# Performance work log

Hardware: AMD Instinct MI355X
Metric: run time of the kernel (lower is better)

The kernel has to match this reference:

```python
import jax, jax.numpy as jnp
import numpy as np

N_NODES = 100000
N_EDGES = 1600000
NUM_GRAPHS = 128
EPS = 1e-5


def setup_inputs() -> dict:
    key = jax.random.key(0)
    ks = jax.random.split(key, 8)
    x = jax.random.normal(ks[0], (N_NODES, 8), dtype=jnp.float32)
    edge_index = jax.random.randint(ks[1], (2, N_EDGES), 0, N_NODES, dtype=jnp.int64)
    batch = jnp.sort(jax.random.randint(ks[2], (N_NODES,), 0, NUM_GRAPHS, dtype=jnp.int64))
    W1_l = jax.random.normal(ks[3], (128, 8), dtype=jnp.float32) * 0.3
    b1 = jnp.zeros((128,), dtype=jnp.float32)
    W1_r = jax.random.normal(ks[4], (128, 8), dtype=jnp.float32) * 0.3
    g1 = jnp.ones((128,), dtype=jnp.float32)
    beta1 = jnp.zeros((128,), dtype=jnp.float32)
    W2_l = jax.random.normal(ks[5], (128, 128), dtype=jnp.float32) * 0.08
    b2 = jnp.zeros((128,), dtype=jnp.float32)
    W2_r = jax.random.normal(ks[6], (128, 128), dtype=jnp.float32) * 0.08
    g2 = jnp.ones((128,), dtype=jnp.float32)
    beta2 = jnp.zeros((128,), dtype=jnp.float32)
    return dict(x=x, edge_index=edge_index, batch=batch,
                W1_l=W1_l, b1=b1, W1_r=W1_r, g1=g1, beta1=beta1,
                W2_l=W2_l, b2=b2, W2_r=W2_r, g2=g2, beta2=beta2)


def _sage_conv(x, src, dst, W_l, b, W_r):
    # PyG SAGEConv: out = lin_l(mean_j x_j) + lin_r(x_i); lin_r has no bias
    msg = x[src]                                              # [E, F]
    agg = jax.ops.segment_sum(msg, dst, num_segments=N_NODES)
    deg = jax.ops.segment_sum(jnp.ones((src.shape[0],), x.dtype), dst,
                              num_segments=N_NODES)
    agg = agg / jnp.maximum(deg, 1.0)[:, None]                # mean aggregation
    return agg @ W_l.T + b + x @ W_r.T


def _batch_norm(h, gamma, beta):
    # training-mode BN over the node dimension
    mu = jnp.mean(h, axis=0)
    var = jnp.mean(jnp.square(h - mu), axis=0)
    return gamma * (h - mu) * jax.lax.rsqrt(var + EPS) + beta


def reference(x, edge_index, batch, W1_l, b1, W1_r, g1, beta1,
              W2_l, b2, W2_r, g2, beta2):
    src, dst = edge_index[0], edge_index[1]
    x1 = jax.nn.relu(_batch_norm(_sage_conv(x, src, dst, W1_l, b1, W1_r), g1, beta1))
    x2 = jax.nn.relu(_batch_norm(_sage_conv(x1, src, dst, W2_l, b2, W2_r), g2, beta2))
    h = x1 + x2  # dropout is identity in eval mode
    # global mean pool per graph
    s = jax.ops.segment_sum(h, batch, num_segments=NUM_GRAPHS)
    cnt = jax.ops.segment_sum(jnp.ones((h.shape[0],), h.dtype), batch,
                              num_segments=NUM_GRAPHS)
    return s / jnp.maximum(cnt, 1.0)[:, None]                 # [NUM_GRAPHS, 128]
```

## Files before the change

### kernel.cpp

```cpp
#include <hip/hip_runtime.h>
#include <cstdint>
#include <cstddef>

namespace {

constexpr int N_NODES = 100000;
constexpr int N_EDGES = 1600000;
constexpr int NUM_GRAPHS = 128;
constexpr int F = 128;
constexpr float BN_EPS = 1e-5f;

constexpr int W_BUCK = 512;
constexpr int NBUCK = (N_NODES + W_BUCK - 1) / W_BUCK;
constexpr int CB = 400;
constexpr int CHUNK = N_EDGES / CB;

typedef float f32x4 __attribute__((ext_vector_type(4)));
typedef float f32x2 __attribute__((ext_vector_type(2)));
typedef short s16x8 __attribute__((ext_vector_type(8)));
typedef unsigned char uchar;
union B8 { uint4 u; s16x8 s; };

__device__ inline ushort f2bf(float x) {
    uint u = __float_as_uint(x);
    u += 0x7fffu + ((u >> 16) & 1u);
    return (ushort)(u >> 16);
}
__device__ inline float bf2f(ushort s) { return __uint_as_float(((uint)s) << 16); }
__device__ inline uint pack2(float lo, float hi) {
    return (uint)f2bf(lo) | ((uint)f2bf(hi) << 16);
}
__device__ inline float bflo(uint u) { return __uint_as_float(u << 16); }
__device__ inline float bfhi(uint u) { return __uint_as_float(u & 0xffff0000u); }

__device__ inline void acc4f8(float* a, uint u) {
    f32x2 lo = __builtin_amdgcn_cvt_pk_f32_fp8((int)u, false);
    f32x2 hi = __builtin_amdgcn_cvt_pk_f32_fp8((int)u, true);
    a[0] += lo[0]; a[1] += lo[1]; a[2] += hi[0]; a[3] += hi[1];
}
__device__ inline void acc8bf(float* a, uint4 v) {
    a[0] += bflo(v.x); a[1] += bfhi(v.x);
    a[2] += bflo(v.y); a[3] += bfhi(v.y);
    a[4] += bflo(v.z); a[5] += bfhi(v.z);
    a[6] += bflo(v.w); a[7] += bfhi(v.w);
}


constexpr int PB_HIST  = CB;
constexpr int PB_BOUND = (N_NODES + 255) / 256;
constexpr int PB_PB    = 64;
constexpr int PB_PB1   = 16;
constexpr int PB_PX    = (N_NODES + 255) / 256;
constexpr int PB_Z     = (512 + NUM_GRAPHS * F) / 256;
constexpr int PB_TOTAL = PB_HIST + PB_BOUND + PB_PB + PB_PB1 + PB_PX + PB_Z;

__global__ void __launch_bounds__(256) k_pre(
        const int* __restrict__ ei, int* __restrict__ gcount,
        const int* __restrict__ batch, int* __restrict__ gstart,
        const float* __restrict__ W2l, const float* __restrict__ W2r,
        ushort* __restrict__ Wcat,
        const float* __restrict__ W1l, const float* __restrict__ W1r,
        ushort* __restrict__ Wcat1,
        const float* __restrict__ x, ushort* __restrict__ xbf,
        float* __restrict__ stats, float* __restrict__ outacc) {
    __shared__ int bins[NBUCK];
    int bid = blockIdx.x, t = threadIdx.x;
    if (bid < PB_HIST) {
        for (int i = t; i < NBUCK; i += 256) bins[i] = 0;
        __syncthreads();
        int e0 = bid * CHUNK;
        for (int i = t; i < CHUNK; i += 256)
            atomicAdd(&bins[ei[N_EDGES + e0 + i] >> 9], 1);
        __syncthreads();
        for (int i = t; i < NBUCK; i += 256) gcount[i * CB + bid] = bins[i];
        return;
    }
    bid -= PB_HIST;
    if (bid < PB_BOUND) {
        int i = bid * 256 + t;
        if (i >= N_NODES) return;
        int b = batch[i];
        if (i == 0) {
            for (int g = 0; g <= b; ++g) gstart[g] = 0;
        } else {
            int p = batch[i - 1];
            if (p != b) for (int g = p + 1; g <= b; ++g) gstart[g] = i;
        }
        if (i == N_NODES - 1) {
            for (int g = b + 1; g <= NUM_GRAPHS; ++g) gstart[g] = N_NODES;
        }
        return;
    }
    bid -= PB_BOUND;
    if (bid < PB_PB) {
        int i = bid * 256 + t;
        int f = i >> 7, k = i & 127;
        Wcat[f * 256 + k]       = f2bf(W2l[i]);
        Wcat[f * 256 + 128 + k] = f2bf(W2r[i]);
        return;
    }
    bid -= PB_PB;
    if (bid < PB_PB1) {
        int i = bid * 256 + t;
        int f = i >> 5, k = i & 31;
        float v = (k < 8) ? W1r[f * 8 + k] : ((k < 16) ? W1l[f * 8 + (k - 8)] : 0.f);
        Wcat1[i] = f2bf(v);
        return;
    }
    bid -= PB_PB1;
    if (bid < PB_PX) {
        int n = bid * 256 + t;
        if (n >= N_NODES) return;
        const float4* xp = (const float4*)(x + (size_t)n * 8);
        float4 x0 = xp[0], x1 = xp[1];
        uint4 o = {pack2(x0.x, x0.y), pack2(x0.z, x0.w),
                   pack2(x1.x, x1.y), pack2(x1.z, x1.w)};
        *(uint4*)(xbf + (size_t)n * 8) = o;
        return;
    }
    bid -= PB_PX;
    {
        int i = bid * 256 + t;
        if (i < 512) stats[i] = 0.f;
        else outacc[i - 512] = 0.f;
    }
}


__global__ void __launch_bounds__(512) k_scanA(int* __restrict__ g,
                                               int* __restrict__ bsum) {
    __shared__ int tmp[512];
    int b = blockIdx.x, t = threadIdx.x;
    int v = (t < CB) ? g[b * CB + t] : 0;
    tmp[t] = v;
    __syncthreads();
    #pragma unroll
    for (int d = 1; d < 512; d <<= 1) {
        int u = (t >= d) ? tmp[t - d] : 0;
        __syncthreads();
        tmp[t] += u;
        __syncthreads();
    }
    if (t < CB) g[b * CB + t] = tmp[t] - v;
    if (t == 511) bsum[b] = tmp[511];
}

__global__ void __launch_bounds__(256) k_part(const int* __restrict__ ei,
                                              const int* __restrict__ gloc,
                                              const int* __restrict__ bsum,
                                              uint* __restrict__ epk) {
    __shared__ int cur[NBUCK];
    __shared__ int pref[256];
    int t = threadIdx.x;
    int v = (t < NBUCK) ? bsum[t] : 0;
    pref[t] = v;
    __syncthreads();
    #pragma unroll
    for (int d = 1; d < 256; d <<= 1) {
        int u = (t >= d) ? pref[t - d] : 0;
        __syncthreads();
        pref[t] += u;
        __syncthreads();
    }
    if (t < NBUCK) cur[t] = gloc[t * CB + blockIdx.x] + (pref[t] - v);
    __syncthreads();
    int e0 = blockIdx.x * CHUNK;
    for (int i = t; i < CHUNK; i += 256) {
        int d = ei[N_EDGES + e0 + i];
        int s = ei[e0 + i];
        int p = atomicAdd(&cur[d >> 9], 1);
        epk[p] = ((uint)s << 9) | (uint)(d & 511);
    }
}

__global__ void __launch_bounds__(512) k_rank(const uint* __restrict__ epk,
                                              const int* __restrict__ bsum,
                                              int* __restrict__ offs,
                                              int* __restrict__ ssrc,
                                              const float* __restrict__ x,
                                              const ushort* __restrict__ xbf,
                                              ushort* __restrict__ xa) {
    __shared__ int dcnt[W_BUCK];
    __shared__ int tmp[W_BUCK];
    __shared__ int cur[W_BUCK];
    __shared__ int pref[256];
    int b = blockIdx.x, t = threadIdx.x;
    if (t < 256) pref[t] = (t < NBUCK) ? bsum[t] : 0;
    __syncthreads();
    #pragma unroll
    for (int d = 1; d < 256; d <<= 1) {
        int u = (t < 256 && t >= d) ? pref[t - d] : 0;
        __syncthreads();
        if (t < 256) pref[t] += u;
        __syncthreads();
    }
    int s0 = pref[b] - bsum[b];
    int s1 = pref[b];
    dcnt[t] = 0;
    __syncthreads();
    for (int i = s0 + t; i < s1; i += 512)
        atomicAdd(&dcnt[epk[i] & 511u], 1);
    __syncthreads();
    int v = dcnt[t];
    tmp[t] = v;
    __syncthreads();
    #pragma unroll
    for (int d = 1; d < 512; d <<= 1) {
        int u = (t >= d) ? tmp[t - d] : 0;
        __syncthreads();
        tmp[t] += u;
        __syncthreads();
    }
    int start = s0 + tmp[t] - v;
    int node = b * W_BUCK + t;
    if (node <= N_NODES) offs[node] = start;
    cur[t] = start;
    __syncthreads();
    for (int i = s0 + t; i < s1; i += 512) {
        uint u = epk[i];
        int p = atomicAdd(&cur[u & 511u], 1);
        ssrc[p] = (int)(u >> 9);
    }

    __syncthreads();
    if (node >= N_NODES) return;
    int gs = start, ge = start + v;
    float a[8];
    #pragma unroll
    for (int i = 0; i < 8; ++i) a[i] = 0.f;
    int j = gs;
    for (; j + 7 < ge; j += 8) {
        int i0 = ssrc[j],   i1 = ssrc[j+1], i2 = ssrc[j+2], i3 = ssrc[j+3];
        int i4 = ssrc[j+4], i5 = ssrc[j+5], i6 = ssrc[j+6], i7 = ssrc[j+7];
        uint4 v0 = *(const uint4*)(xbf + (size_t)i0 * 8);
        uint4 v1 = *(const uint4*)(xbf + (size_t)i1 * 8);
        uint4 v2 = *(const uint4*)(xbf + (size_t)i2 * 8);
        uint4 v3 = *(const uint4*)(xbf + (size_t)i3 * 8);
        uint4 v4 = *(const uint4*)(xbf + (size_t)i4 * 8);
        uint4 v5 = *(const uint4*)(xbf + (size_t)i5 * 8);
        uint4 v6 = *(const uint4*)(xbf + (size_t)i6 * 8);
        uint4 v7 = *(const uint4*)(xbf + (size_t)i7 * 8);
        acc8bf(a, v0); acc8bf(a, v1); acc8bf(a, v2); acc8bf(a, v3);
        acc8bf(a, v4); acc8bf(a, v5); acc8bf(a, v6); acc8bf(a, v7);
    }
    for (; j + 3 < ge; j += 4) {
        int i0 = ssrc[j], i1 = ssrc[j+1], i2 = ssrc[j+2], i3 = ssrc[j+3];
        uint4 v0 = *(const uint4*)(xbf + (size_t)i0 * 8);
        uint4 v1 = *(const uint4*)(xbf + (size_t)i1 * 8);
        uint4 v2 = *(const uint4*)(xbf + (size_t)i2 * 8);
        uint4 v3 = *(const uint4*)(xbf + (size_t)i3 * 8);
        acc8bf(a, v0); acc8bf(a, v1); acc8bf(a, v2); acc8bf(a, v3);
    }
    for (; j < ge; ++j)
        acc8bf(a, *(const uint4*)(xbf + (size_t)ssrc[j] * 8));
    int dg = ge - gs;
    float inv = 1.0f / (float)(dg > 1 ? dg : 1);
    const float4* xp = (const float4*)(x + (size_t)node * 8);
    float4 x0 = xp[0], x1v = xp[1];
    ushort* row = xa + (size_t)node * 32;
    uint4 o0 = {pack2(x0.x, x0.y), pack2(x0.z, x0.w), pack2(x1v.x, x1v.y), pack2(x1v.z, x1v.w)};
    uint4 o1 = {pack2(a[0]*inv, a[1]*inv), pack2(a[2]*inv, a[3]*inv),
                pack2(a[4]*inv, a[5]*inv), pack2(a[6]*inv, a[7]*inv)};
    uint4 z = {0u, 0u, 0u, 0u};
    *(uint4*)(row)      = o0;
    *(uint4*)(row + 8)  = o1;
    *(uint4*)(row + 16) = z;
    *(uint4*)(row + 24) = z;
}


__global__ void __launch_bounds__(256) k_lin1(
        const ushort* __restrict__ xa, const ushort* __restrict__ Wcat1,
        const float* __restrict__ b1, ushort* __restrict__ h1bf,
        float* __restrict__ stats) {
    __shared__ ushort sOut[64 * 140];
    __shared__ float sred[256];
    int tid = threadIdx.x;
    int wave = tid >> 6, lane = tid & 63;
    int quad = lane >> 4, l16 = lane & 15;
    int n0 = blockIdx.x * 64;

    int node = n0 + wave * 16 + l16;
    int cn = (node < N_NODES) ? node : N_NODES - 1;
    B8 ta;
    ta.u = *(const uint4*)(xa + (size_t)cn * 32 + quad * 8);

    #pragma unroll
    for (int nt = 0; nt < 8; ++nt) {
        int fb = nt * 16 + l16;
        B8 tb;
        tb.u = *(const uint4*)(Wcat1 + fb * 32 + quad * 8);
        f32x4 acc = {0.f, 0.f, 0.f, 0.f};
        acc = __builtin_amdgcn_mfma_f32_16x16x32_bf16(ta.s, tb.s, acc, 0, 0, 0);
        float bb = b1[fb];
        #pragma unroll
        for (int r = 0; r < 4; ++r) {
            int row = wave * 16 + quad * 4 + r;
            sOut[row * 140 + fb] = f2bf(acc[r] + bb);
        }
    }
    __syncthreads();

    #pragma unroll
    for (int p = 0; p < 4; ++p) {
        int row = p * 16 + (tid >> 4);
        int nd = n0 + row;
        if (nd < N_NODES) {
            int c0 = (tid & 15) * 8;
            uint4 v = *(const uint4*)&sOut[row * 140 + c0];
            *(uint4*)(h1bf + (size_t)nd * F + c0) = v;
        }
    }

    int f = tid & 127, half = tid >> 7;
    float s = 0.f, s2 = 0.f;
    for (int r = half * 32; r < half * 32 + 32; ++r) {
        if (n0 + r >= N_NODES) break;
        float v = bf2f(sOut[r * 140 + f]);
        s += v; s2 += v * v;
    }
    if (half) { sred[f] = s; sred[128 + f] = s2; }
    __syncthreads();
    if (!half) {
        s += sred[f]; s2 += sred[128 + f];
        atomicAdd(&stats[f], s);
        atomicAdd(&stats[F + f], s2);
    }
}

__global__ void k_bnrelu(const ushort* __restrict__ h, const float* __restrict__ stats,
                         const float* __restrict__ gamma, const float* __restrict__ beta,
                         ushort* __restrict__ x1bf, uchar* __restrict__ x1f8) {
    int i = blockIdx.x * 256 + threadIdx.x;
    int base = i * 8;
    int f = base & (F - 1);
    float sc[8], sh[8];
    #pragma unroll
    for (int k = 0; k < 8; ++k) {
        float mu  = stats[f + k] * (1.0f / N_NODES);
        float var = stats[F + f + k] * (1.0f / N_NODES) - mu * mu;
        float s   = gamma[f + k] * rsqrtf(var + BN_EPS);
        sc[k] = s;
        sh[k] = beta[f + k] - mu * s;
    }
    uint4 hv = *(const uint4*)(h + base);
    float v0 = fmaxf(0.f, bflo(hv.x)*sc[0] + sh[0]);
    float v1 = fmaxf(0.f, bfhi(hv.x)*sc[1] + sh[1]);
    float v2 = fmaxf(0.f, bflo(hv.y)*sc[2] + sh[2]);
    float v3 = fmaxf(0.f, bfhi(hv.y)*sc[3] + sh[3]);
    float v4 = fmaxf(0.f, bflo(hv.z)*sc[4] + sh[4]);
    float v5 = fmaxf(0.f, bfhi(hv.z)*sc[5] + sh[5]);
    float v6 = fmaxf(0.f, bflo(hv.w)*sc[6] + sh[6]);
    float v7 = fmaxf(0.f, bfhi(hv.w)*sc[7] + sh[7]);
    uint4 o = {pack2(v0,v1), pack2(v2,v3), pack2(v4,v5), pack2(v6,v7)};
    *(uint4*)(x1bf + base) = o;
    int p0 = __builtin_amdgcn_cvt_pk_fp8_f32(v0, v1, 0, false);
    p0     = __builtin_amdgcn_cvt_pk_fp8_f32(v2, v3, p0, true);
    int p1 = __builtin_amdgcn_cvt_pk_fp8_f32(v4, v5, 0, false);
    p1     = __builtin_amdgcn_cvt_pk_fp8_f32(v6, v7, p1, true);
    uint2 o8 = {(uint)p0, (uint)p1};
    *(uint2*)(x1f8 + base) = o8;
}


__global__ void __launch_bounds__(256) k_agg2(
        const uchar* __restrict__ x1f8, const int* __restrict__ offs,
        const int* __restrict__ ssrc, ushort* __restrict__ agg2bf) {
    int t = threadIdx.x;
    int n = blockIdx.x * 32 + (t >> 3);
    int c16 = (t & 7) * 16;
    int s0 = offs[n], s1 = offs[n + 1];
    float acc[16];
    #pragma unroll
    for (int i = 0; i < 16; ++i) acc[i] = 0.f;
    int j = s0;
    for (; j + 7 < s1; j += 8) {
        int i0 = ssrc[j],   i1 = ssrc[j+1], i2 = ssrc[j+2], i3 = ssrc[j+3];
        int i4 = ssrc[j+4], i5 = ssrc[j+5], i6 = ssrc[j+6], i7 = ssrc[j+7];
        uint4 v0 = *(const uint4*)(x1f8 + (size_t)i0 * F + c16);
        uint4 v1 = *(const uint4*)(x1f8 + (size_t)i1 * F + c16);
        uint4 v2 = *(const uint4*)(x1f8 + (size_t)i2 * F + c16);
        uint4 v3 = *(const uint4*)(x1f8 + (size_t)i3 * F + c16);
        uint4 v4 = *(const uint4*)(x1f8 + (size_t)i4 * F + c16);
        uint4 v5 = *(const uint4*)(x1f8 + (size_t)i5 * F + c16);
        uint4 v6 = *(const uint4*)(x1f8 + (size_t)i6 * F + c16);
        uint4 v7 = *(const uint4*)(x1f8 + (size_t)i7 * F + c16);
        acc4f8(acc, v0.x); acc4f8(acc+4, v0.y); acc4f8(acc+8, v0.z); acc4f8(acc+12, v0.w);
        acc4f8(acc, v1.x); acc4f8(acc+4, v1.y); acc4f8(acc+8, v1.z); acc4f8(acc+12, v1.w);
        acc4f8(acc, v2.x); acc4f8(acc+4, v2.y); acc4f8(acc+8, v2.z); acc4f8(acc+12, v2.w);
        acc4f8(acc, v3.x); acc4f8(acc+4, v3.y); acc4f8(acc+8, v3.z); acc4f8(acc+12, v3.w);
        acc4f8(acc, v4.x); acc4f8(acc+4, v4.y); acc4f8(acc+8, v4.z); acc4f8(acc+12, v4.w);
        acc4f8(acc, v5.x); acc4f8(acc+4, v5.y); acc4f8(acc+8, v5.z); acc4f8(acc+12, v5.w);
        acc4f8(acc, v6.x); acc4f8(acc+4, v6.y); acc4f8(acc+8, v6.z); acc4f8(acc+12, v6.w);
        acc4f8(acc, v7.x); acc4f8(acc+4, v7.y); acc4f8(acc+8, v7.z); acc4f8(acc+12, v7.w);
    }
    for (; j + 3 < s1; j += 4) {
        int i0 = ssrc[j], i1 = ssrc[j+1], i2 = ssrc[j+2], i3 = ssrc[j+3];
        uint4 v0 = *(const uint4*)(x1f8 + (size_t)i0 * F + c16);
        uint4 v1 = *(const uint4*)(x1f8 + (size_t)i1 * F + c16);
        uint4 v2 = *(const uint4*)(x1f8 + (size_t)i2 * F + c16);
        uint4 v3 = *(const uint4*)(x1f8 + (size_t)i3 * F + c16);
        acc4f8(acc, v0.x); acc4f8(acc+4, v0.y); acc4f8(acc+8, v0.z); acc4f8(acc+12, v0.w);
        acc4f8(acc, v1.x); acc4f8(acc+4, v1.y); acc4f8(acc+8, v1.z); acc4f8(acc+12, v1.w);
        acc4f8(acc, v2.x); acc4f8(acc+4, v2.y); acc4f8(acc+8, v2.z); acc4f8(acc+12, v2.w);
        acc4f8(acc, v3.x); acc4f8(acc+4, v3.y); acc4f8(acc+8, v3.z); acc4f8(acc+12, v3.w);
    }
    for (; j < s1; ++j) {
        uint4 v = *(const uint4*)(x1f8 + (size_t)ssrc[j] * F + c16);
        acc4f8(acc, v.x); acc4f8(acc+4, v.y); acc4f8(acc+8, v.z); acc4f8(acc+12, v.w);
    }
    int dg = s1 - s0;
    float inv = 1.0f / (float)(dg > 1 ? dg : 1);
    uint4 o0 = {pack2(acc[0]*inv,  acc[1]*inv),  pack2(acc[2]*inv,  acc[3]*inv),
                pack2(acc[4]*inv,  acc[5]*inv),  pack2(acc[6]*inv,  acc[7]*inv)};
    uint4 o1 = {pack2(acc[8]*inv,  acc[9]*inv),  pack2(acc[10]*inv, acc[11]*inv),
                pack2(acc[12]*inv, acc[13]*inv), pack2(acc[14]*inv, acc[15]*inv)};
    ushort* dst = agg2bf + (size_t)n * F + c16;
    *(uint4*)(dst)     = o0;
    *(uint4*)(dst + 8) = o1;
}

__device__ inline int gSw(int f, int j) { return (f << 5) | ((j + f) & 31); }

__global__ void __launch_bounds__(256, 2) k_lin2(
        const ushort* __restrict__ agg2bf, const ushort* __restrict__ x1bf,
        const ushort* __restrict__ Wcat, const float* __restrict__ b2,
        ushort* __restrict__ h2bf, float* __restrict__ stats) {
    __shared__ ushort sB[2048 * 8];
    int tid = threadIdx.x;
    int wave = tid >> 6, lane = tid & 63;
    int quad = lane >> 4, l16 = lane & 15;

    int bid = blockIdx.x;
    int ng, fh;
    if (bid < 768) {
        int g = bid >> 4, i = bid & 15;
        ng = g * 8 + (i & 7);
        fh = i >> 3;
    } else {
        int idx = bid - 768;
        ng = 384 + (idx >> 1);
        fh = idx & 1;
    }
    int fbase = fh * 64;
    int wf = wave & 1, grp = wave >> 1;
    int f0 = wf * 32 + l16;
    int f1 = f0 + 16;

    #pragma unroll
    for (int it = 0; it < 8; ++it) {
        int c = it * 256 + tid;
        int f = c >> 5, j = c & 31;
        uint4 v = *(const uint4*)(Wcat + ((size_t)(fbase + f) * 32 + j) * 8);
        *(uint4*)&sB[gSw(f, j) * 8] = v;
    }
    __syncthreads();

    float bb0 = b2[fbase + f0], bb1 = b2[fbase + f1];
    float s0 = 0.f, s0q = 0.f, s1 = 0.f, s1q = 0.f;
    int n0 = ng * 256 + grp * 128;

    s16x8 aA[8], aB[8];
    auto loadTile = [&](s16x8* a, int nb) {
        int an = nb + l16;
        if (an >= N_NODES) an = N_NODES - 1;
        #pragma unroll
        for (int ks = 0; ks < 8; ++ks) {
            const ushort* src = (ks < 4) ? agg2bf : x1bf;
            B8 tm;
            tm.u = *(const uint4*)(src + (size_t)an * F + (ks & 3) * 32 + quad * 8);
            a[ks] = tm.s;
        }
    };
    auto computeTile = [&](s16x8* a, int nb) {
        f32x4 acc0 = {0,0,0,0}, acc1 = {0,0,0,0};
        #pragma unroll
        for (int ks = 0; ks < 8; ++ks) {
            int j = (ks << 2) + quad;
            B8 tb0, tb1;
            tb0.u = *(const uint4*)&sB[gSw(f0, j) * 8];
            tb1.u = *(const uint4*)&sB[gSw(f1, j) * 8];
            acc0 = __builtin_amdgcn_mfma_f32_16x16x32_bf16(a[ks], tb0.s, acc0, 0, 0, 0);
            acc1 = __builtin_amdgcn_mfma_f32_16x16x32_bf16(a[ks], tb1.s, acc1, 0, 0, 0);
        }
        #pragma unroll
        for (int r = 0; r < 4; ++r) {
            int node = nb + quad * 4 + r;
            if (node < N_NODES) {
                float v0 = acc0[r] + bb0, v1 = acc1[r] + bb1;
                h2bf[(size_t)node * F + fbase + f0] = f2bf(v0);
                h2bf[(size_t)node * F + fbase + f1] = f2bf(v1);
                s0 += v0; s0q += v0 * v0;
                s1 += v1; s1q += v1 * v1;
            }
        }
    };

    loadTile(aA, n0);
    #pragma unroll 1
    for (int p = 0; p < 4; ++p) {
        int nb = n0 + p * 32;
        loadTile(aB, nb + 16);
        computeTile(aA, nb);
        if (p < 3) loadTile(aA, nb + 32);
        computeTile(aB, nb + 16);
    }

    s0  += __shfl_xor(s0, 16);  s0  += __shfl_xor(s0, 32);
    s0q += __shfl_xor(s0q, 16); s0q += __shfl_xor(s0q, 32);
    s1  += __shfl_xor(s1, 16);  s1  += __shfl_xor(s1, 32);
    s1q += __shfl_xor(s1q, 16); s1q += __shfl_xor(s1q, 32);
    if (quad == 0) {
        atomicAdd(&stats[fbase + f0], s0);
        atomicAdd(&stats[F + fbase + f0], s0q);
        atomicAdd(&stats[fbase + f1], s1);
        atomicAdd(&stats[F + fbase + f1], s1q);
    }
}


__global__ void k_pool(const ushort* __restrict__ x1bf, const ushort* __restrict__ h2bf,
                       const float* __restrict__ stats2, const float* __restrict__ gamma2,
                       const float* __restrict__ beta2, const int* __restrict__ batch,
                       float* __restrict__ outacc) {
    int f = threadIdx.x & 127;
    int half = threadIdx.x >> 7;
    float mu  = stats2[f] * (1.0f / N_NODES);
    float var = stats2[F + f] * (1.0f / N_NODES) - mu * mu;
    float sc  = gamma2[f] * rsqrtf(var + BN_EPS);
    float sh  = beta2[f] - mu * sc;
    int n0 = blockIdx.x * 128 + half * 64;
    if (n0 >= N_NODES) return;
    int n1 = min(n0 + 64, N_NODES);
    float acc = 0.f;
    int curg = batch[n0];
    for (int n = n0; n < n1; ++n) {
        int g = batch[n];
        if (g != curg) {
            atomicAdd(&outacc[curg * F + f], acc);
            acc = 0.f; curg = g;
        }
        float v1 = bf2f(x1bf[(size_t)n * F + f]);
        float v2 = fmaxf(0.f, bf2f(h2bf[(size_t)n * F + f]) * sc + sh);
        acc += v1 + v2;
    }
    atomicAdd(&outacc[curg * F + f], acc);
}

__global__ void k_out(const float* __restrict__ outacc, const int* __restrict__ gstart,
                      float* __restrict__ out) {
    int i = blockIdx.x * 256 + threadIdx.x;
    if (i >= NUM_GRAPHS * F) return;
    int g = i >> 7;
    int c = gstart[g + 1] - gstart[g];
    out[i] = outacc[i] / (float)(c > 1 ? c : 1);
}

}

extern "C" void kernel_launch(void* const* d_in, const int* in_sizes, int n_in,
                              void* d_out, int out_size, void* d_ws, size_t ws_size,
                              hipStream_t stream) {
    const float* x     = (const float*)d_in[0];
    const int*   ei    = (const int*)d_in[1];
    const int*   batch = (const int*)d_in[2];
    const float* W1l   = (const float*)d_in[3];
    const float* b1    = (const float*)d_in[4];
    const float* W1r   = (const float*)d_in[5];
    const float* g1    = (const float*)d_in[6];
    const float* be1   = (const float*)d_in[7];
    const float* W2l   = (const float*)d_in[8];
    const float* b2    = (const float*)d_in[9];
    const float* W2r   = (const float*)d_in[10];
    const float* g2    = (const float*)d_in[11];
    const float* be2   = (const float*)d_in[12];
    float* out = (float*)d_out;

    char* w = (char*)d_ws;
    size_t o = 0;
    auto alloc = [&](size_t bytes) {
        void* p = w + o;
        o += (bytes + 511) & ~(size_t)511;
        return p;
    };
    int*    offs   = (int*)alloc((size_t)(N_NODES + 1) * 4);
    int*    gcount = (int*)alloc((size_t)NBUCK * CB * 4);
    int*    bsum   = (int*)alloc((size_t)NBUCK * 4);
    int*    ssrc   = (int*)alloc((size_t)N_EDGES * 4);
    uint*   epk    = (uint*)alloc((size_t)N_EDGES * 4);
    int*    gstart = (int*)alloc((NUM_GRAPHS + 1) * 4);
    float*  stats  = (float*)alloc(512 * 4);
    ushort* Wcat   = (ushort*)alloc((size_t)F * 256 * 2);
    ushort* Wcat1  = (ushort*)alloc((size_t)F * 32 * 2);
    float*  outacc = (float*)alloc((size_t)NUM_GRAPHS * F * 4);
    ushort* xbf    = (ushort*)alloc((size_t)N_NODES * 8 * 2);
    ushort* xa     = (ushort*)alloc((size_t)N_NODES * 32 * 2);
    ushort* h1bf   = (ushort*)alloc((size_t)N_NODES * F * 2);
    ushort* x1bf   = (ushort*)alloc((size_t)N_NODES * F * 2);
    uchar*  x1f8   = (uchar*)alloc((size_t)N_NODES * F);
    ushort* agg2bf = (ushort*)alloc((size_t)N_NODES * F * 2);
    ushort* h2bf   = (ushort*)alloc((size_t)N_NODES * F * 2);

    k_pre<<<PB_TOTAL, 256, 0, stream>>>(ei, gcount, batch, gstart,
                                        W2l, W2r, Wcat, W1l, W1r, Wcat1,
                                        x, xbf, stats, outacc);

    k_scanA<<<NBUCK, 512, 0, stream>>>(gcount, bsum);
    k_part <<<CB, 256, 0, stream>>>(ei, gcount, bsum, epk);
    k_rank <<<NBUCK, 512, 0, stream>>>(epk, bsum, offs, ssrc, x, xbf, xa);

    k_lin1  <<<(N_NODES + 63) / 64, 256, 0, stream>>>(xa, Wcat1, b1, h1bf, stats);
    k_bnrelu<<<(N_NODES * F / 8) / 256, 256, 0, stream>>>(h1bf, stats, g1, be1,
                                                          x1bf, x1f8);

    k_agg2  <<<N_NODES / 32, 256, 0, stream>>>(x1f8, offs, ssrc, agg2bf);
    k_lin2  <<<((N_NODES + 255) / 256) * 2, 256, 0, stream>>>(agg2bf, x1bf, Wcat, b2,
                                                              h2bf, stats + 256);

    k_pool<<<(N_NODES + 127) / 128, 256, 0, stream>>>(x1bf, h2bf, stats + 256,
                                                      g2, be2, batch, outacc);
    k_out <<<(NUM_GRAPHS * F + 255) / 256, 256, 0, stream>>>(outacc, gstart, out);
}
```

Measured before the change: 308.2 us.

## Recompute layer-1 linear to fuse BN+ReLU and drop h1 intermediate buffer

Splits layer-1 linear into a stats-only pass and a second pass that recomputes the cheap K=32 MFMA, then applies BN, ReLU and the bf16/fp8 conversion directly. This removes the write and re-read of the 25.6MB bf16 h1 intermediate and the separate k_bnrelu kernel. It trades that memory traffic for a second read of xa and a duplicated matmul, plus shared-memory atomics for the stats reduction.

```diff
diff --git a/kernel.cpp b/kernel.cpp
--- a/kernel.cpp
+++ b/kernel.cpp
@@ -269,16 +269,16 @@
 }
 
 
-__global__ void __launch_bounds__(256) k_lin1(
+__global__ void __launch_bounds__(256) k_lin1s(
         const ushort* __restrict__ xa, const ushort* __restrict__ Wcat1,
-        const float* __restrict__ b1, ushort* __restrict__ h1bf,
-        float* __restrict__ stats) {
-    __shared__ ushort sOut[64 * 140];
+        const float* __restrict__ b1, float* __restrict__ stats) {
     __shared__ float sred[256];
     int tid = threadIdx.x;
     int wave = tid >> 6, lane = tid & 63;
     int quad = lane >> 4, l16 = lane & 15;
     int n0 = blockIdx.x * 64;
+    sred[tid] = 0.f;
+    __syncthreads();
 
     int node = n0 + wave * 16 + l16;
     int cn = (node < N_NODES) ? node : N_NODES - 1;
@@ -293,10 +293,60 @@
         f32x4 acc = {0.f, 0.f, 0.f, 0.f};
         acc = __builtin_amdgcn_mfma_f32_16x16x32_bf16(ta.s, tb.s, acc, 0, 0, 0);
         float bb = b1[fb];
+        float ls = 0.f, lq = 0.f;
+        #pragma unroll
+        for (int r = 0; r < 4; ++r) {
+            int rn = n0 + wave * 16 + quad * 4 + r;
+            if (rn < N_NODES) {
+                float v = bf2f(f2bf(acc[r] + bb));
+                ls += v; lq += v * v;
+            }
+        }
+        ls += __shfl_xor(ls, 16); ls += __shfl_xor(ls, 32);
+        lq += __shfl_xor(lq, 16); lq += __shfl_xor(lq, 32);
+        if (quad == 0) {
+            atomicAdd(&sred[fb], ls);
+            atomicAdd(&sred[128 + fb], lq);
+        }
+    }
+    __syncthreads();
+    atomicAdd(&stats[tid], sred[tid]);
+}
+
+__global__ void __launch_bounds__(256) k_lin1b(
+        const ushort* __restrict__ xa, const ushort* __restrict__ Wcat1,
+        const float* __restrict__ b1, const float* __restrict__ stats,
+        const float* __restrict__ gamma, const float* __restrict__ beta,
+        ushort* __restrict__ x1bf, uchar* __restrict__ x1f8) {
+    __shared__ ushort sOut[64 * 140];
+    int tid = threadIdx.x;
+    int wave = tid >> 6, lane = tid & 63;
+    int quad = lane >> 4, l16 = lane & 15;
+    int n0 = blockIdx.x * 64;
+
+    int node = n0 + wave * 16 + l16;
+    int cn = (node < N_NODES) ? node : N_NODES - 1;
+    B8 ta;
+    ta.u = *(const uint4*)(xa + (size_t)cn * 32 + quad * 8);
+
+    #pragma unroll
+    for (int nt = 0; nt < 8; ++nt) {
+        int fb = nt * 16 + l16;
+        B8 tb;
+        tb.u = *(const uint4*)(Wcat1 + fb * 32 + quad * 8);
+        f32x4 acc = {0.f, 0.f, 0.f, 0.f};
+        acc = __builtin_amdgcn_mfma_f32_16x16x32_bf16(ta.s, tb.s, acc, 0, 0, 0);
+        float bb = b1[fb];
+        float mu  = stats[fb] * (1.0f / N_NODES);
+        float var = stats[F + fb] * (1.0f / N_NODES) - mu * mu;
+        float sc  = gamma[fb] * rsqrtf(var + BN_EPS);
+        float sh  = beta[fb] - mu * sc;
         #pragma unroll
         for (int r = 0; r < 4; ++r) {
             int row = wave * 16 + quad * 4 + r;
-            sOut[row * 140 + fb] = f2bf(acc[r] + bb);
+            float v = bf2f(f2bf(acc[r] + bb));
+            float y = fmaxf(0.f, v * sc + sh);
+            sOut[row * 140 + fb] = f2bf(y);
         }
     }
     __syncthreads();
@@ -308,58 +358,17 @@
         if (nd < N_NODES) {
             int c0 = (tid & 15) * 8;
             uint4 v = *(const uint4*)&sOut[row * 140 + c0];
-            *(uint4*)(h1bf + (size_t)nd * F + c0) = v;
-        }
-    }
-
-    int f = tid & 127, half = tid >> 7;
-    float s = 0.f, s2 = 0.f;
-    for (int r = half * 32; r < half * 32 + 32; ++r) {
-        if (n0 + r >= N_NODES) break;
-        float v = bf2f(sOut[r * 140 + f]);
-        s += v; s2 += v * v;
-    }
-    if (half) { sred[f] = s; sred[128 + f] = s2; }
-    __syncthreads();
-    if (!half) {
-        s += sred[f]; s2 += sred[128 + f];
-        atomicAdd(&stats[f], s);
-        atomicAdd(&stats[F + f], s2);
-    }
-}
-
-__global__ void k_bnrelu(const ushort* __restrict__ h, const float* __restrict__ stats,
-                         const float* __restrict__ gamma, const float* __restrict__ beta,
-                         ushort* __restrict__ x1bf, uchar* __restrict__ x1f8) {
-    int i = blockIdx.x * 256 + threadIdx.x;
-    int base = i * 8;
-    int f = base & (F - 1);
-    float sc[8], sh[8];
-    #pragma unroll
-    for (int k = 0; k < 8; ++k) {
-        float mu  = stats[f + k] * (1.0f / N_NODES);
-        float var = stats[F + f + k] * (1.0f / N_NODES) - mu * mu;
-        float s   = gamma[f + k] * rsqrtf(var + BN_EPS);
-        sc[k] = s;
-        sh[k] = beta[f + k] - mu * s;
-    }
-    uint4 hv = *(const uint4*)(h + base);
-    float v0 = fmaxf(0.f, bflo(hv.x)*sc[0] + sh[0]);
-    float v1 = fmaxf(0.f, bfhi(hv.x)*sc[1] + sh[1]);
-    float v2 = fmaxf(0.f, bflo(hv.y)*sc[2] + sh[2]);
-    float v3 = fmaxf(0.f, bfhi(hv.y)*sc[3] + sh[3]);
-    float v4 = fmaxf(0.f, bflo(hv.z)*sc[4] + sh[4]);
-    float v5 = fmaxf(0.f, bfhi(hv.z)*sc[5] + sh[5]);
-    float v6 = fmaxf(0.f, bflo(hv.w)*sc[6] + sh[6]);
-    float v7 = fmaxf(0.f, bfhi(hv.w)*sc[7] + sh[7]);
-    uint4 o = {pack2(v0,v1), pack2(v2,v3), pack2(v4,v5), pack2(v6,v7)};
-    *(uint4*)(x1bf + base) = o;
-    int p0 = __builtin_amdgcn_cvt_pk_fp8_f32(v0, v1, 0, false);
-    p0     = __builtin_amdgcn_cvt_pk_fp8_f32(v2, v3, p0, true);
-    int p1 = __builtin_amdgcn_cvt_pk_fp8_f32(v4, v5, 0, false);
-    p1     = __builtin_amdgcn_cvt_pk_fp8_f32(v6, v7, p1, true);
-    uint2 o8 = {(uint)p0, (uint)p1};
-    *(uint2*)(x1f8 + base) = o8;
+            *(uint4*)(x1bf + (size_t)nd * F + c0) = v;
+            float f0 = bflo(v.x), f1 = bfhi(v.x), f2 = bflo(v.y), f3 = bfhi(v.y);
+            float f4 = bflo(v.z), f5 = bfhi(v.z), f6 = bflo(v.w), f7 = bfhi(v.w);
+            int p0 = __builtin_amdgcn_cvt_pk_fp8_f32(f0, f1, 0, false);
+            p0     = __builtin_amdgcn_cvt_pk_fp8_f32(f2, f3, p0, true);
+            int p1 = __builtin_amdgcn_cvt_pk_fp8_f32(f4, f5, 0, false);
+            p1     = __builtin_amdgcn_cvt_pk_fp8_f32(f6, f7, p1, true);
+            uint2 o8 = {(uint)p0, (uint)p1};
+            *(uint2*)(x1f8 + (size_t)nd * F + c0) = o8;
+        }
+    }
 }
 
 
@@ -595,7 +604,6 @@
     float*  outacc = (float*)alloc((size_t)NUM_GRAPHS * F * 4);
     ushort* xbf    = (ushort*)alloc((size_t)N_NODES * 8 * 2);
     ushort* xa     = (ushort*)alloc((size_t)N_NODES * 32 * 2);
-    ushort* h1bf   = (ushort*)alloc((size_t)N_NODES * F * 2);
     ushort* x1bf   = (ushort*)alloc((size_t)N_NODES * F * 2);
     uchar*  x1f8   = (uchar*)alloc((size_t)N_NODES * F);
     ushort* agg2bf = (ushort*)alloc((size_t)N_NODES * F * 2);
@@ -609,9 +617,9 @@
     k_part <<<CB, 256, 0, stream>>>(ei, gcount, bsum, epk);
     k_rank <<<NBUCK, 512, 0, stream>>>(epk, bsum, offs, ssrc, x, xbf, xa);
 
-    k_lin1  <<<(N_NODES + 63) / 64, 256, 0, stream>>>(xa, Wcat1, b1, h1bf, stats);
-    k_bnrelu<<<(N_NODES * F / 8) / 256, 256, 0, stream>>>(h1bf, stats, g1, be1,
-                                                          x1bf, x1f8);
+    k_lin1s<<<(N_NODES + 63) / 64, 256, 0, stream>>>(xa, Wcat1, b1, stats);
+    k_lin1b<<<(N_NODES + 63) / 64, 256, 0, stream>>>(xa, Wcat1, b1, stats,
+                                                     g1, be1, x1bf, x1f8);
 
     k_agg2  <<<N_NODES / 32, 256, 0, stream>>>(x1f8, offs, ssrc, agg2bf);
     k_lin2  <<<((N_NODES + 255) / 256) * 2, 256, 0, stream>>>(agg2bf, x1bf, Wcat, b2,
```

Measured after the change: 310.1 us. About the same (+0.6%).
